# Performance work log

Measured on AMD Instinct MI355X. Metric: run time of the kernel, lower is better.

## Reference

```python
import jax, jax.numpy as jnp
import numpy as np

B, L, S, D = 16, 32, 128, 256
WIN = 9
NEG = -1e10
EPS = 1e-6


def _band_mask(seq_len, win_size):
    half = win_size // 2
    i = jnp.arange(seq_len)
    m = jnp.abs(i[:, None] - i[None, :]) <= half
    return m[None, None, :, :]


def setup_inputs() -> dict:
    key = jax.random.key(0)
    ks = jax.random.split(key, 12)
    H_s = jax.random.normal(ks[0], (B, L, S, D), dtype=jnp.float32)
    seg_mask = jnp.ones((B, L, 1, S), dtype=bool)
    s = 0.02
    return {
        "H_s": H_s,
        "seg_mask": seg_mask,
        "Wq": jax.random.normal(ks[1], (D, D), jnp.float32) * s,
        "Wk": jax.random.normal(ks[2], (D, D), jnp.float32) * s,
        "Wv": jax.random.normal(ks[3], (D, D), jnp.float32) * s,
        "Wh_w": jax.random.normal(ks[4], (D, 1), jnp.float32) * s,
        "Wh_b": jnp.zeros((1,), jnp.float32),
        "Wg_w": jax.random.normal(ks[5], (D, 1), jnp.float32) * s,
        "Wl_w": jax.random.normal(ks[6], (D, 1), jnp.float32) * s,
        "ln_g": jnp.ones((D,), jnp.float32),
        "ln_b": jnp.zeros((D,), jnp.float32),
        "feat_simi": _band_mask(S, WIN),
    }


def reference(H_s, seg_mask, Wq, Wk, Wv, Wh_w, Wh_b, Wg_w, Wl_w, ln_g, ln_b, feat_simi):
    d = H_s.shape[-1]
    scaling = jnp.asarray(d, H_s.dtype) ** 0.5
    Q = H_s @ Wq
    K = H_s @ Wk
    V = H_s @ Wv
    # shared scores, computed once: (B, L, S, S)
    GP = jnp.einsum('blqd,blkd->blqk', Q / scaling, K)
    GP = jnp.where(seg_mask, GP, NEG)  # global path mask
    G_Att = jnp.einsum('blqk,blkd->blqd', jax.nn.softmax(GP, axis=-1), V)
    LP = jnp.where(feat_simi, GP, NEG)  # local window mask on top
    L_Att = jnp.einsum('blqk,blkd->blqd', jax.nn.softmax(LP, axis=-1), V)
    gate = jax.nn.sigmoid((H_s @ Wh_w + Wh_b) + G_Att @ Wg_w + L_Att @ Wl_w)
    Fusion = gate * L_Att + (1.0 - gate) * G_Att
    x = Fusion + H_s
    mu = jnp.mean(x, axis=-1, keepdims=True)
    var = jnp.var(x, axis=-1, keepdims=True)
    return ln_g * (x - mu) / jnp.sqrt(var + EPS) + ln_b
```

## Files before the change

### kernel.cpp

```cpp
#include <hip/hip_runtime.h>
#include <hip/hip_bf16.h>
#include <stdint.h>


#define NBL   512
#define SS    128
#define DD    256
#define BLKT  512
#define QSTR  264
#define VSTR  136
#define WSTR  40
#define NEGF  (-1e10f)

#define OFF_Q   0
#define OFF_KV  (SS * QSTR * 2)
#define OFF_WT  (OFF_KV + DD * VSTR * 2)
#define OFF_W5  (OFF_WT + DD * WSTR * 2)
#define SMEM_BYTES (OFF_W5 + 5 * DD * 4)

typedef __attribute__((ext_vector_type(8))) short bf16x8;
typedef __attribute__((ext_vector_type(4))) float floatx4;

__device__ __forceinline__ uint32_t f2bf1(float f) {
  uint32_t u = __float_as_uint(f);
  return (u + 0x7fffu + ((u >> 16) & 1u)) >> 16;
}
__device__ __forceinline__ short f2bs(float f) { return (short)f2bf1(f); }
__device__ __forceinline__ uint32_t packbf(float a, float b) {
  return f2bf1(a) | (f2bf1(b) << 16);
}
__device__ __forceinline__ float qredSum(float v) {
  v += __shfl_xor(v, 1, 64); v += __shfl_xor(v, 2, 64);
  v += __shfl_xor(v, 4, 64); v += __shfl_xor(v, 8, 64);
  return v;
}
__device__ __forceinline__ float qredMax(float v) {
  v = fmaxf(v, __shfl_xor(v, 1, 64)); v = fmaxf(v, __shfl_xor(v, 2, 64));
  v = fmaxf(v, __shfl_xor(v, 4, 64)); v = fmaxf(v, __shfl_xor(v, 8, 64));
  return v;
}

template <int TR>
__device__ __forceinline__ void proj_mfma(const bf16x8* __restrict__ a,
                                          const float* __restrict__ W,
                                          uint16_t* __restrict__ dst, int dstStride,
                                          uint16_t* __restrict__ sWT,
                                          int tid, int m0, int n, int quad) {
  floatx4 acc[16];
#pragma unroll
  for (int i = 0; i < 16; ++i) acc[i] = (floatx4){0.f, 0.f, 0.f, 0.f};
  const int sd  = tid & 255;
  const int eb0 = tid >> 8;
  float wbuf[2][16];

#define LD_SLICE(B, KS)                                           \
  {                                                               \
    _Pragma("unroll")                                             \
    for (int i = 0; i < 4; ++i) {                                 \
      const int ge = (KS) * 32 + (eb0 + 2 * i) * 4;               \
      _Pragma("unroll")                                           \
      for (int j = 0; j < 4; ++j)                                 \
        wbuf[B][i * 4 + j] = W[(ge + j) * DD + sd];               \
    }                                                             \
  }

  LD_SLICE(0, 0);
#pragma unroll
  for (int ks = 0; ks < 8; ++ks) {
    if (ks < 7) LD_SLICE((ks + 1) & 1, ks + 1);
    __syncthreads();
#pragma unroll
    for (int i = 0; i < 4; ++i) {
      const int e = (eb0 + 2 * i) * 4;
      const float* wp = &wbuf[ks & 1][i * 4];
      *(uint2*)(sWT + sd * WSTR + e) = make_uint2(packbf(wp[0], wp[1]), packbf(wp[2], wp[3]));
    }
    __syncthreads();
#pragma unroll
    for (int nt = 0; nt < 16; ++nt) {
      const bf16x8 b = *(const bf16x8*)(sWT + (nt * 16 + n) * WSTR + quad * 8);
      acc[nt] = __builtin_amdgcn_mfma_f32_16x16x32_bf16(a[ks], b, acc[nt], 0, 0, 0);
    }
  }
#undef LD_SLICE

#pragma unroll
  for (int nt = 0; nt < 16; ++nt) {
    if (TR == 0) {
#pragma unroll
      for (int r = 0; r < 4; ++r)
        dst[(m0 + quad * 4 + r) * dstStride + nt * 16 + n] = (uint16_t)f2bf1(acc[nt][r]);
    } else {
      *(uint2*)(dst + (nt * 16 + n) * dstStride + m0 + quad * 4) =
          make_uint2(packbf(acc[nt][0], acc[nt][1]), packbf(acc[nt][2], acc[nt][3]));
    }
  }
}

__global__ __launch_bounds__(BLKT, 2) void segatt_kernel(
    const float* __restrict__ Hs, const float* __restrict__ Wq,
    const float* __restrict__ Wk, const float* __restrict__ Wv,
    const float* __restrict__ Whw, const float* __restrict__ Whb,
    const float* __restrict__ Wgw, const float* __restrict__ Wlw,
    const float* __restrict__ lng, const float* __restrict__ lnb,
    float* __restrict__ Out) {
  extern __shared__ __align__(16) char smem[];
  uint16_t* sQ  = (uint16_t*)(smem + OFF_Q);
  uint16_t* sK  = (uint16_t*)(smem + OFF_KV);
  uint16_t* sVT = (uint16_t*)(smem + OFF_KV);
  uint16_t* sWT = (uint16_t*)(smem + OFF_WT);
  float*    sW5 = (float*)(smem + OFF_W5);

  const int tid  = threadIdx.x;
  const int bl   = blockIdx.x;
  const int lane = tid & 63;
  const int n    = lane & 15;
  const int quad = lane >> 4;
  const int m0   = (tid >> 6) * 16;
  const float* Hbl = Hs + (size_t)bl * SS * DD;
  float*       Obl = Out + (size_t)bl * SS * DD;
  const float Whb0 = Whb[0];

  for (int i = tid; i < 5 * DD; i += BLKT) {
    const int j = i & (DD - 1);
    const int m = i >> 8;
    sW5[i] = (m == 0) ? Whw[j] : (m == 1) ? Wgw[j] : (m == 2) ? Wlw[j]
           : (m == 3) ? lng[j] : lnb[j];
  }

  bf16x8 a[8];
#pragma unroll
  for (int ks = 0; ks < 8; ++ks) {
    const float* hp = Hbl + (m0 + n) * DD + ks * 32 + quad * 8;
    const float4 h0 = *(const float4*)hp;
    const float4 h1 = *(const float4*)(hp + 4);
    a[ks][0] = f2bs(h0.x); a[ks][1] = f2bs(h0.y); a[ks][2] = f2bs(h0.z); a[ks][3] = f2bs(h0.w);
    a[ks][4] = f2bs(h1.x); a[ks][5] = f2bs(h1.y); a[ks][6] = f2bs(h1.z); a[ks][7] = f2bs(h1.w);
  }

  proj_mfma<0>(a, Wq, sQ, QSTR, sWT, tid, m0, n, quad);
  proj_mfma<0>(a, Wk, sK, QSTR, sWT, tid, m0, n, quad);
  __syncthreads();

  {
    floatx4 gp[8];
#pragma unroll
    for (int i = 0; i < 8; ++i) gp[i] = (floatx4){0.f, 0.f, 0.f, 0.f};
    for (int ks = 0; ks < 8; ++ks) {
      const bf16x8 aq = *(const bf16x8*)(sQ + (m0 + n) * QSTR + ks * 32 + quad * 8);
#pragma unroll
      for (int nt = 0; nt < 8; ++nt) {
        const bf16x8 bk = *(const bf16x8*)(sK + (nt * 16 + n) * QSTR + ks * 32 + quad * 8);
        gp[nt] = __builtin_amdgcn_mfma_f32_16x16x32_bf16(aq, bk, gp[nt], 0, 0, 0);
      }
    }
#pragma unroll
    for (int r = 0; r < 4; ++r) {
      const int q = m0 + quad * 4 + r;
      float g[8], e[8];
      float vm = -3.0e38f;
#pragma unroll
      for (int nt = 0; nt < 8; ++nt) { g[nt] = gp[nt][r] * 0.0625f; vm = fmaxf(vm, g[nt]); }
      const float rm = qredMax(vm);
      float s = 0.f;
#pragma unroll
      for (int nt = 0; nt < 8; ++nt) { e[nt] = __expf(g[nt] - rm); s += e[nt]; }
      const float inv = 1.f / qredSum(s);
      uint16_t* row = sQ + q * QSTR;
#pragma unroll
      for (int nt = 0; nt < 8; ++nt) row[nt * 16 + n] = (uint16_t)f2bf1(e[nt] * inv);
      float lvm = -3.0e38f;
#pragma unroll
      for (int nt = 0; nt < 8; ++nt) {
        const int kk = nt * 16 + n;
        int dk = q - kk; if (dk < 0) dk = -dk;
        g[nt] = (dk <= 4) ? g[nt] : NEGF;
        lvm = fmaxf(lvm, g[nt]);
      }
      const float lm = qredMax(lvm);
      float ls = 0.f;
#pragma unroll
      for (int nt = 0; nt < 8; ++nt) { e[nt] = __expf(g[nt] - lm); ls += e[nt]; }
      const float linv = 1.f / qredSum(ls);
#pragma unroll
      for (int nt = 0; nt < 8; ++nt) row[128 + nt * 16 + n] = (uint16_t)f2bf1(e[nt] * linv);
    }
  }
  __syncthreads();

  proj_mfma<1>(a, Wv, sVT, VSTR, sWT, tid, m0, n, quad);
  __syncthreads();

  {
    floatx4 ag[16], al[16];
#pragma unroll
    for (int i = 0; i < 16; ++i) {
      ag[i] = (floatx4){0.f, 0.f, 0.f, 0.f};
      al[i] = (floatx4){0.f, 0.f, 0.f, 0.f};
    }
    for (int ks = 0; ks < 4; ++ks) {
      const bf16x8 ap = *(const bf16x8*)(sQ + (m0 + n) * QSTR + ks * 32 + quad * 8);
#pragma unroll
      for (int nt = 0; nt < 16; ++nt) {
        const bf16x8 bv = *(const bf16x8*)(sVT + (nt * 16 + n) * VSTR + ks * 32 + quad * 8);
        ag[nt] = __builtin_amdgcn_mfma_f32_16x16x32_bf16(ap, bv, ag[nt], 0, 0, 0);
      }
    }
    int sLo = m0 - 4;  if (sLo < 0) sLo = 0;
    int sHi = m0 + 19; if (sHi > SS - 1) sHi = SS - 1;
    for (int ks = sLo >> 5; ks <= (sHi >> 5); ++ks) {
      const bf16x8 ap = *(const bf16x8*)(sQ + (m0 + n) * QSTR + 128 + ks * 32 + quad * 8);
#pragma unroll
      for (int nt = 0; nt < 16; ++nt) {
        const bf16x8 bv = *(const bf16x8*)(sVT + (nt * 16 + n) * VSTR + ks * 32 + quad * 8);
        al[nt] = __builtin_amdgcn_mfma_f32_16x16x32_bf16(ap, bv, al[nt], 0, 0, 0);
      }
    }
#pragma unroll
    for (int r = 0; r < 4; ++r) {
      const int q = m0 + quad * 4 + r;
      const float* Hrow = Hbl + q * DD + n;
      float hv[16];
      float part = 0.f;
#pragma unroll
      for (int nt = 0; nt < 16; ++nt) {
        hv[nt] = Hrow[nt * 16];
        const int d = nt * 16 + n;
        part += hv[nt] * sW5[d] + ag[nt][r] * sW5[256 + d] + al[nt][r] * sW5[512 + d];
      }
      const float tot  = qredSum(part) + Whb0;
      const float gate = 1.f / (1.f + __expf(-tot));
      float s = 0.f, ss = 0.f;
#pragma unroll
      for (int nt = 0; nt < 16; ++nt) {
        const float x = gate * al[nt][r] + (1.f - gate) * ag[nt][r] + hv[nt];
        s += x; ss += x * x;
      }
      s = qredSum(s); ss = qredSum(ss);
      const float mu   = s * (1.f / 256.f);
      const float var  = ss * (1.f / 256.f) - mu * mu;
      const float rstd = rsqrtf(var + 1e-6f);
      float* Orow = Obl + q * DD + n;
#pragma unroll
      for (int nt = 0; nt < 16; ++nt) {
        const int d = nt * 16 + n;
        const float x = gate * al[nt][r] + (1.f - gate) * ag[nt][r] + hv[nt];
        Orow[nt * 16] = sW5[768 + d] * (x - mu) * rstd + sW5[1024 + d];
      }
    }
  }
}

extern "C" void kernel_launch(void* const* d_in, const int* in_sizes, int n_in,
                              void* d_out, int out_size, void* d_ws, size_t ws_size,
                              hipStream_t stream) {
  const float* Hs  = (const float*)d_in[0];
  const float* Wq  = (const float*)d_in[2];
  const float* Wk  = (const float*)d_in[3];
  const float* Wv  = (const float*)d_in[4];
  const float* Whw = (const float*)d_in[5];
  const float* Whb = (const float*)d_in[6];
  const float* Wgw = (const float*)d_in[7];
  const float* Wlw = (const float*)d_in[8];
  const float* lng = (const float*)d_in[9];
  const float* lnb = (const float*)d_in[10];
  float* Out = (float*)d_out;

  (void)hipFuncSetAttribute((const void*)segatt_kernel,
                            hipFuncAttributeMaxDynamicSharedMemorySize, SMEM_BYTES);
  segatt_kernel<<<dim3(NBL), dim3(BLKT), SMEM_BYTES, stream>>>(
      Hs, Wq, Wk, Wv, Whw, Whb, Wgw, Wlw, lng, lnb, Out);
}
```

Baseline: 233.0 us.

## Double-buffer weight slices in LDS to halve barriers per projection step

Replaces the single LDS weight-transpose buffer (two barriers per k-step) with two ping-pong buffers aliased onto the K/V region, so each k-step needs one barrier. Barriers become a raw lgkmcnt wait plus s_barrier instead of __syncthreads, and the dedicated weight buffer is removed, shrinking LDS use. Because the buffers alias sK/sVT, extra guard barriers are added around the output writes. The risks are race conditions from the aliasing and the weaker barrier, which does not wait on vmcnt.

Result: slower. 238.5 us (+2.4%).

```diff
diff --git a/kernel.cpp b/kernel.cpp
--- a/kernel.cpp
+++ b/kernel.cpp
@@ -12,11 +12,12 @@
 #define WSTR  40
 #define NEGF  (-1e10f)
 
-#define OFF_Q   0
-#define OFF_KV  (SS * QSTR * 2)
-#define OFF_WT  (OFF_KV + DD * VSTR * 2)
-#define OFF_W5  (OFF_WT + DD * WSTR * 2)
+#define OFF_Q    0
+#define OFF_KV   (SS * QSTR * 2)
+#define KV_BYTES (DD * VSTR * 2)
+#define OFF_W5   (OFF_KV + KV_BYTES)
 #define SMEM_BYTES (OFF_W5 + 5 * DD * 4)
+#define BUF_BYTES (DD * WSTR * 2)
 
 typedef __attribute__((ext_vector_type(8))) short bf16x8;
 typedef __attribute__((ext_vector_type(4))) float floatx4;
@@ -40,49 +41,63 @@
   return v;
 }
 
-template <int TR>
-__device__ __forceinline__ void proj_mfma(const bf16x8* __restrict__ a,
+#define LBAR() asm volatile("s_waitcnt lgkmcnt(0)\n\ts_barrier" ::: "memory")
+
+#define LD_SLICE(DST, KS)                                          \
+  {                                                                \
+    _Pragma("unroll")                                              \
+    for (int i = 0; i < 4; ++i) {                                  \
+      const int ge = (KS) * 32 + (eb0 + 2 * i) * 4;                \
+      _Pragma("unroll")                                            \
+      for (int j = 0; j < 4; ++j)                                  \
+        (DST)[i * 4 + j] = W[(ge + j) * DD + gd];                  \
+    }                                                              \
+  }
+
+#define ST_SLICE(BUF, SRC)                                         \
+  {                                                                \
+    _Pragma("unroll")                                              \
+    for (int i = 0; i < 4; ++i) {                                  \
+      const int e = (eb0 + 2 * i) * 4;                             \
+      *(uint2*)((BUF) + gd * WSTR + e) =                           \
+          make_uint2(packbf((SRC)[i * 4 + 0], (SRC)[i * 4 + 1]),   \
+                     packbf((SRC)[i * 4 + 2], (SRC)[i * 4 + 3]));  \
+    }                                                              \
+  }
+
+#define PITER(KS, CURW, NXTW, CURBUF)                              \
+  {                                                                \
+    if ((KS) < 7) LD_SLICE(NXTW, (KS) + 1);                        \
+    ST_SLICE(CURBUF, CURW);                                        \
+    LBAR();                                                        \
+    _Pragma("unroll")                                              \
+    for (int nt = 0; nt < 16; ++nt) {                              \
+      const bf16x8 b = *(const bf16x8*)((CURBUF) + (nt * 16 + n) * WSTR + quad * 8); \
+      acc[nt] = __builtin_amdgcn_mfma_f32_16x16x32_bf16(a[KS], b, acc[nt], 0, 0, 0); \
+    }                                                              \
+  }
+
+template <int TR, bool GUARD>
+__device__ __forceinline__ void proj_pipe(const bf16x8* __restrict__ a,
                                           const float* __restrict__ W,
                                           uint16_t* __restrict__ dst, int dstStride,
-                                          uint16_t* __restrict__ sWT,
+                                          uint16_t* __restrict__ buf0,
+                                          uint16_t* __restrict__ buf1,
                                           int tid, int m0, int n, int quad) {
   floatx4 acc[16];
 #pragma unroll
   for (int i = 0; i < 16; ++i) acc[i] = (floatx4){0.f, 0.f, 0.f, 0.f};
-  const int sd  = tid & 255;
+  const int gd  = tid & 255;
   const int eb0 = tid >> 8;
-  float wbuf[2][16];
-
-#define LD_SLICE(B, KS)                                           \
-  {                                                               \
-    _Pragma("unroll")                                             \
-    for (int i = 0; i < 4; ++i) {                                 \
-      const int ge = (KS) * 32 + (eb0 + 2 * i) * 4;               \
-      _Pragma("unroll")                                           \
-      for (int j = 0; j < 4; ++j)                                 \
-        wbuf[B][i * 4 + j] = W[(ge + j) * DD + sd];               \
-    }                                                             \
-  }
-
-  LD_SLICE(0, 0);
-#pragma unroll
-  for (int ks = 0; ks < 8; ++ks) {
-    if (ks < 7) LD_SLICE((ks + 1) & 1, ks + 1);
-    __syncthreads();
-#pragma unroll
-    for (int i = 0; i < 4; ++i) {
-      const int e = (eb0 + 2 * i) * 4;
-      const float* wp = &wbuf[ks & 1][i * 4];
-      *(uint2*)(sWT + sd * WSTR + e) = make_uint2(packbf(wp[0], wp[1]), packbf(wp[2], wp[3]));
-    }
-    __syncthreads();
-#pragma unroll
-    for (int nt = 0; nt < 16; ++nt) {
-      const bf16x8 b = *(const bf16x8*)(sWT + (nt * 16 + n) * WSTR + quad * 8);
-      acc[nt] = __builtin_amdgcn_mfma_f32_16x16x32_bf16(a[ks], b, acc[nt], 0, 0, 0);
-    }
-  }
-#undef LD_SLICE
+  float wA[16], wB[16];
+
+  LD_SLICE(wA, 0);
+  PITER(0, wA, wB, buf0)  PITER(1, wB, wA, buf1)
+  PITER(2, wA, wB, buf0)  PITER(3, wB, wA, buf1)
+  PITER(4, wA, wB, buf0)  PITER(5, wB, wA, buf1)
+  PITER(6, wA, wB, buf0)  PITER(7, wB, wA, buf1)
+
+  if (GUARD) LBAR();
 
 #pragma unroll
   for (int nt = 0; nt < 16; ++nt) {
@@ -95,6 +110,7 @@
           make_uint2(packbf(acc[nt][0], acc[nt][1]), packbf(acc[nt][2], acc[nt][3]));
     }
   }
+  if (GUARD) LBAR();
 }
 
 __global__ __launch_bounds__(BLKT, 2) void segatt_kernel(
@@ -105,11 +121,12 @@
     const float* __restrict__ lng, const float* __restrict__ lnb,
     float* __restrict__ Out) {
   extern __shared__ __align__(16) char smem[];
-  uint16_t* sQ  = (uint16_t*)(smem + OFF_Q);
-  uint16_t* sK  = (uint16_t*)(smem + OFF_KV);
-  uint16_t* sVT = (uint16_t*)(smem + OFF_KV);
-  uint16_t* sWT = (uint16_t*)(smem + OFF_WT);
-  float*    sW5 = (float*)(smem + OFF_W5);
+  uint16_t* sQ   = (uint16_t*)(smem + OFF_Q);
+  uint16_t* sK   = (uint16_t*)(smem + OFF_KV);
+  uint16_t* sVT  = (uint16_t*)(smem + OFF_KV);
+  uint16_t* buf0 = (uint16_t*)(smem + OFF_KV);
+  uint16_t* buf1 = (uint16_t*)(smem + OFF_KV + BUF_BYTES);
+  float*    sW5  = (float*)(smem + OFF_W5);
 
   const int tid  = threadIdx.x;
   const int bl   = blockIdx.x;
@@ -138,9 +155,8 @@
     a[ks][4] = f2bs(h1.x); a[ks][5] = f2bs(h1.y); a[ks][6] = f2bs(h1.z); a[ks][7] = f2bs(h1.w);
   }
 
-  proj_mfma<0>(a, Wq, sQ, QSTR, sWT, tid, m0, n, quad);
-  proj_mfma<0>(a, Wk, sK, QSTR, sWT, tid, m0, n, quad);
-  __syncthreads();
+  proj_pipe<0, false>(a, Wq, sQ, QSTR, buf0, buf1, tid, m0, n, quad);
+  proj_pipe<0, true >(a, Wk, sK, QSTR, buf0, buf1, tid, m0, n, quad);
 
   {
     floatx4 gp[8];
@@ -186,10 +202,9 @@
       for (int nt = 0; nt < 8; ++nt) row[128 + nt * 16 + n] = (uint16_t)f2bf1(e[nt] * linv);
     }
   }
-  __syncthreads();
-
-  proj_mfma<1>(a, Wv, sVT, VSTR, sWT, tid, m0, n, quad);
-  __syncthreads();
+  LBAR();
+
+  proj_pipe<1, true>(a, Wv, sVT, VSTR, buf0, buf1, tid, m0, n, quad);
 
   {
     floatx4 ag[16], al[16];
```
